# Kernel tuning notes

Measured on AMD Instinct MI355X. Metric: run time of the kernel, lower is better.

## Reference

```python
import jax, jax.numpy as jnp
import numpy as np

M, L, O, D, B = 512, 16, 32, 64, 16
GAMMA = 1.0 / (2.0 * D)  # RBF bandwidth ~ median sq-dist of randn data


def _rbf(X, Y):
    """Gaussian RBF kernel. X:[M,D]; Y:[M2,D] -> [M,M2] or Y:[B,L,D] -> [B,M,L]."""
    x2 = jnp.sum(X * X, axis=-1)
    y2 = jnp.sum(Y * Y, axis=-1)
    if Y.ndim == 3:
        d2 = x2[None, :, None] + y2[:, None, :] - 2.0 * jnp.einsum('md,bld->bml', X, Y)
    else:
        d2 = x2[:, None] + y2[None, :] - 2.0 * X @ Y.T
    return jnp.exp(-GAMMA * d2)


def setup_inputs() -> dict:
    key = jax.random.key(0)
    k1, k2, k3, k4 = jax.random.split(key, 4)
    inps = jax.random.normal(k1, (B, L, D), dtype=jnp.float32)
    nys_X = jax.random.normal(k2, (M, D), dtype=jnp.float32)
    nys_Y = jax.random.normal(k3, (M, D), dtype=jnp.float32)
    # xavier_uniform for (M*L, M*L)
    lim = float(np.sqrt(6.0 / (2 * M * L)))
    koopman = jax.random.uniform(k4, (M * L, M * L), dtype=jnp.float32, minval=-lim, maxval=lim)
    return {"inps": inps, "nys_X": nys_X, "nys_Y": nys_Y, "koopman": koopman}


def reference(inps, nys_X, nys_Y, koopman):
    scale = M ** (-0.5)
    KX = _rbf(nys_X, inps) * scale   # [B, M, L]
    KY = _rbf(nys_Y, nys_Y) * scale  # [M, M]
    out0 = KX.reshape(B, M * L)      # [B, M*L]

    def step(carry, _):
        nxt = carry @ koopman.T      # einsum('ij,bj->bi', G, out)
        return nxt, nxt

    _, outs = jax.lax.scan(step, out0, None, length=O)   # [O, B, M*L]
    outs = jnp.transpose(outs, (1, 2, 0)).reshape(B, M, L, O)
    outs = jnp.einsum('ij,bjlo->bilo', KY, outs)          # [B, M, L, O]
    outs = jnp.einsum('ja,bjlo->bloa', nys_Y, outs)       # [B, L, O, D]
    return outs
```

## Files before the change

kernel.cpp:

```cpp
#include <hip/hip_runtime.h>
#include <hip/hip_bf16.h>

#define M_  512
#define L_  16
#define O_  32
#define D_  64
#define B_  16
#define ML  8192
#define SLOT (B_*ML)

typedef __attribute__((ext_vector_type(8))) short short8;
typedef __attribute__((ext_vector_type(4))) float f32x4;

static constexpr float GAMMA = 1.0f / 128.0f;
static constexpr float SCALE = 0.0441941738241592f;

__device__ __forceinline__ float sqdiff4(const float4& x, const float4& y) {
    float dx = x.x - y.x, dy = x.y - y.y, dz = x.z - y.z, dw = x.w - y.w;
    return dx*dx + dy*dy + dz*dz + dw*dw;
}

__device__ __forceinline__ unsigned short f2bf(float x) {
    unsigned u = __float_as_uint(x);
    u = (u + 0x7FFFu + ((u >> 16) & 1u)) >> 16;
    return (unsigned short)u;
}

__global__ __launch_bounds__(256) void k_out0_dual(const float* __restrict__ inps,
                                                   const float* __restrict__ X,
                                                   float* __restrict__ S0,
                                                   unsigned short* __restrict__ C0) {
    int idx = blockIdx.x * 256 + threadIdx.x;
    int l = idx & (L_ - 1);
    int m = (idx >> 4) & (M_ - 1);
    int b = idx >> 13;
    const float* xr = X + m * D_;
    const float* yr = inps + (b * L_ + l) * D_;
    float d2 = 0.f;
#pragma unroll
    for (int d = 0; d < D_; d += 4) {
        float4 xv = *(const float4*)(xr + d);
        float4 yv = *(const float4*)(yr + d);
        d2 += sqdiff4(xv, yv);
    }
    float v = SCALE * expf(-GAMMA * d2);
    S0[idx] = v;
    C0[idx] = f2bf(v);
}

__global__ __launch_bounds__(256) void k_out0(const float* __restrict__ inps,
                                              const float* __restrict__ X,
                                              float* __restrict__ out0) {
    int idx = blockIdx.x * 256 + threadIdx.x;
    int l = idx & (L_ - 1);
    int m = (idx >> 4) & (M_ - 1);
    int b = idx >> 13;
    const float* xr = X + m * D_;
    const float* yr = inps + (b * L_ + l) * D_;
    float d2 = 0.f;
#pragma unroll
    for (int d = 0; d < D_; d += 4) {
        float4 xv = *(const float4*)(xr + d);
        float4 yv = *(const float4*)(yr + d);
        d2 += sqdiff4(xv, yv);
    }
    out0[idx] = SCALE * expf(-GAMMA * d2);
}

__global__ __launch_bounds__(256) void k_ky(const float* __restrict__ Y,
                                            float* __restrict__ KY) {
    int idx = blockIdx.x * 256 + threadIdx.x;
    int j = idx & (M_ - 1);
    int i = idx >> 9;
    const float* yi = Y + i * D_;
    const float* yj = Y + j * D_;
    float d2 = 0.f;
#pragma unroll
    for (int d = 0; d < D_; d += 4) {
        float4 a = *(const float4*)(yi + d);
        float4 b = *(const float4*)(yj + d);
        d2 += sqdiff4(a, b);
    }
    KY[idx] = SCALE * expf(-GAMMA * d2);
}

__global__ __launch_bounds__(256) void k_w(const float* __restrict__ KY,
                                           const float* __restrict__ Y,
                                           float* __restrict__ W) {
    int idx = blockIdx.x * 256 + threadIdx.x;
    int a = idx & (D_ - 1);
    int m = idx >> 6;
    float acc = 0.f;
    for (int j = 0; j < M_; ++j)
        acc = fmaf(KY[m * M_ + j], Y[j * D_ + a], acc);
    W[idx] = acc;
}


__global__ __launch_bounds__(512, 2) void k_step_first(const float* __restrict__ G,
                                                       unsigned short* __restrict__ Gp,
                                                       const unsigned short* __restrict__ Cin,
                                                       float* __restrict__ Sout,
                                                       unsigned short* __restrict__ Cout) {
    const int bx   = blockIdx.x;
    const int w    = threadIdx.x >> 6;
    const int lane = threadIdx.x & 63;
    const int r    = lane & 15;
    const int kk   = lane >> 4;
    const size_t kbase = (size_t)w * 1024 + kk * 8;
    const int mt0 = bx * 2, mt1 = bx * 2 + 1;

    const float* g0 = G + (size_t)(mt0 * 16 + r) * ML + kbase;
    const float* g1 = G + (size_t)(mt1 * 16 + r) * ML + kbase;
    unsigned short* gp0 = Gp + ((size_t)(mt0 * 256 + w * 32) * 64 + lane) * 8;
    unsigned short* gp1 = Gp + ((size_t)(mt1 * 256 + w * 32) * 64 + lane) * 8;
    const unsigned short* bp = Cin + (size_t)r * ML + kbase;

    const bool nt = (w < 4);
    f32x4 acc0 = {0.f, 0.f, 0.f, 0.f};
    f32x4 acc1 = {0.f, 0.f, 0.f, 0.f};
#pragma unroll 2
    for (int it = 0; it < 32; ++it) {
        short8 bv = *(const short8*)(bp + it * 32);
        f32x4 fa = __builtin_nontemporal_load((const f32x4*)(g0 + it * 32));
        f32x4 fb = __builtin_nontemporal_load((const f32x4*)(g0 + it * 32 + 4));
        union { short8 v; unsigned short u[8]; } oa;
        oa.u[0] = f2bf(fa.x); oa.u[1] = f2bf(fa.y); oa.u[2] = f2bf(fa.z); oa.u[3] = f2bf(fa.w);
        oa.u[4] = f2bf(fb.x); oa.u[5] = f2bf(fb.y); oa.u[6] = f2bf(fb.z); oa.u[7] = f2bf(fb.w);
        if (nt) __builtin_nontemporal_store(oa.v, (short8*)(gp0 + (size_t)it * 512));
        else    *(short8*)(gp0 + (size_t)it * 512) = oa.v;
        acc0 = __builtin_amdgcn_mfma_f32_16x16x32_bf16(oa.v, bv, acc0, 0, 0, 0);
        f32x4 fc = __builtin_nontemporal_load((const f32x4*)(g1 + it * 32));
        f32x4 fd = __builtin_nontemporal_load((const f32x4*)(g1 + it * 32 + 4));
        union { short8 v; unsigned short u[8]; } ob;
        ob.u[0] = f2bf(fc.x); ob.u[1] = f2bf(fc.y); ob.u[2] = f2bf(fc.z); ob.u[3] = f2bf(fc.w);
        ob.u[4] = f2bf(fd.x); ob.u[5] = f2bf(fd.y); ob.u[6] = f2bf(fd.z); ob.u[7] = f2bf(fd.w);
        if (nt) __builtin_nontemporal_store(ob.v, (short8*)(gp1 + (size_t)it * 512));
        else    *(short8*)(gp1 + (size_t)it * 512) = ob.v;
        acc1 = __builtin_amdgcn_mfma_f32_16x16x32_bf16(ob.v, bv, acc1, 0, 0, 0);
    }

    __shared__ float red[2][8][256];
    const int rbase = kk << 2;
#pragma unroll
    for (int q = 0; q < 4; ++q) {
        red[0][w][(rbase + q) * 16 + r] = acc0[q];
        red[1][w][(rbase + q) * 16 + r] = acc1[q];
    }
    __syncthreads();

    const int t = threadIdx.x;
    const int tl = t >> 8;
    const int t2 = t & 255;
    float s = 0.f;
#pragma unroll
    for (int p = 0; p < 8; ++p) s += red[tl][p][t2];
    const int b = t2 & 15;
    const int i = (bx << 5) + (tl << 4) + (t2 >> 4);
    Sout[(size_t)b * ML + i] = s;
    Cout[(size_t)b * ML + i] = f2bf(s);
}

template<bool NT>
__device__ __forceinline__ void step_loop(const unsigned short* ap0,
                                          const unsigned short* ap1,
                                          const unsigned short* bp,
                                          f32x4& acc0, f32x4& acc1) {
#pragma unroll 4
    for (int it = 0; it < 32; ++it) {
        short8 bv = *(const short8*)(bp + it * 32);
        short8 a0, a1;
        if constexpr (NT) {
            a0 = __builtin_nontemporal_load((const short8*)(ap0 + (size_t)it * 512));
            a1 = __builtin_nontemporal_load((const short8*)(ap1 + (size_t)it * 512));
        } else {
            a0 = *(const short8*)(ap0 + (size_t)it * 512);
            a1 = *(const short8*)(ap1 + (size_t)it * 512);
        }
        acc0 = __builtin_amdgcn_mfma_f32_16x16x32_bf16(a0, bv, acc0, 0, 0, 0);
        acc1 = __builtin_amdgcn_mfma_f32_16x16x32_bf16(a1, bv, acc1, 0, 0, 0);
    }
}

__global__ __launch_bounds__(512, 4) void k_step_next(const unsigned short* __restrict__ Gp,
                                                      const unsigned short* __restrict__ Cin,
                                                      float* __restrict__ Sout,
                                                      unsigned short* __restrict__ Cout) {
    const int bx   = blockIdx.x;
    const int w    = threadIdx.x >> 6;
    const int lane = threadIdx.x & 63;
    const int r    = lane & 15;
    const int kk   = lane >> 4;
    const size_t kbase = (size_t)w * 1024 + kk * 8;
    const int mt0 = bx * 2, mt1 = bx * 2 + 1;

    const unsigned short* ap0 = Gp + ((size_t)(mt0 * 256 + w * 32) * 64 + lane) * 8;
    const unsigned short* ap1 = Gp + ((size_t)(mt1 * 256 + w * 32) * 64 + lane) * 8;
    const unsigned short* bp  = Cin + (size_t)r * ML + kbase;

    f32x4 acc0 = {0.f, 0.f, 0.f, 0.f};
    f32x4 acc1 = {0.f, 0.f, 0.f, 0.f};
    if (w < 4) step_loop<true >(ap0, ap1, bp, acc0, acc1);
    else       step_loop<false>(ap0, ap1, bp, acc0, acc1);

    __shared__ float red[2][8][256];
    const int rbase = kk << 2;
#pragma unroll
    for (int q = 0; q < 4; ++q) {
        red[0][w][(rbase + q) * 16 + r] = acc0[q];
        red[1][w][(rbase + q) * 16 + r] = acc1[q];
    }
    __syncthreads();

    const int t = threadIdx.x;
    const int tl = t >> 8;
    const int t2 = t & 255;
    float s = 0.f;
#pragma unroll
    for (int p = 0; p < 8; ++p) s += red[tl][p][t2];
    const int b = t2 & 15;
    const int i = (bx << 5) + (tl << 4) + (t2 >> 4);
    Sout[(size_t)b * ML + i] = s;
    Cout[(size_t)b * ML + i] = f2bf(s);
}

__global__ __launch_bounds__(256) void k_step(const float* __restrict__ G,
                                              const float* __restrict__ carry,
                                              float* __restrict__ out) {
    const int i = blockIdx.x;
    const float* __restrict__ grow = G + (size_t)i * ML;
    float acc[B_];
#pragma unroll
    for (int b = 0; b < B_; ++b) acc[b] = 0.f;
    for (int j0 = threadIdx.x * 4; j0 < ML; j0 += 256 * 4) {
        float4 g = *(const float4*)(grow + j0);
#pragma unroll
        for (int b = 0; b < B_; ++b) {
            float4 c = *(const float4*)(carry + b * ML + j0);
            acc[b] = fmaf(g.x, c.x, fmaf(g.y, c.y, fmaf(g.z, c.z, fmaf(g.w, c.w, acc[b]))));
        }
    }
#pragma unroll
    for (int b = 0; b < B_; ++b) {
        float v = acc[b];
#pragma unroll
        for (int off = 32; off > 0; off >>= 1) v += __shfl_down(v, off, 64);
        acc[b] = v;
    }
    __shared__ float red2[4][B_];
    int lane = threadIdx.x & 63;
    int wv   = threadIdx.x >> 6;
    if (lane == 0) {
#pragma unroll
        for (int b = 0; b < B_; ++b) red2[wv][b] = acc[b];
    }
    __syncthreads();
    if (threadIdx.x < B_) {
        float v = red2[0][threadIdx.x] + red2[1][threadIdx.x] +
                  red2[2][threadIdx.x] + red2[3][threadIdx.x];
        out[threadIdx.x * ML + i] = v;
    }
}

__global__ __launch_bounds__(256) void k_final(const float* __restrict__ S,
                                               const float* __restrict__ W,
                                               float* __restrict__ out) {
    int t = blockIdx.x * 256 + threadIdx.x;
    int a = t & (D_ - 1);
    int w = t >> 6;
    int o = w & (O_ - 1);
    int bl = w >> 5;
    int l = bl & (L_ - 1);
    int b = bl >> 4;
    const float* slot = S + (size_t)(o + 1) * SLOT + b * ML;
    float acc = 0.f;
    for (int m = 0; m < M_; ++m)
        acc = fmaf(slot[m * L_ + l], W[m * D_ + a], acc);
    out[t] = acc;
}

extern "C" void kernel_launch(void* const* d_in, const int* in_sizes, int n_in,
                              void* d_out, int out_size, void* d_ws, size_t ws_size,
                              hipStream_t stream) {
    const float* inps    = (const float*)d_in[0];
    const float* nys_X   = (const float*)d_in[1];
    const float* nys_Y   = (const float*)d_in[2];
    const float* koopman = (const float*)d_in[3];
    float* out = (float*)d_out;

    const size_t GB_BYTES  = (size_t)ML * ML * 2;
    const size_t S_BYTES   = (size_t)33 * SLOT * 4;
    const size_t CB_BYTES  = (size_t)33 * SLOT * 2;
    const size_t KY_BYTES  = (size_t)M_ * M_ * 4;
    const size_t W_BYTES   = (size_t)M_ * D_ * 4;
    const size_t NEED_FAST = GB_BYTES + S_BYTES + CB_BYTES + KY_BYTES + W_BYTES;

    if (ws_size >= NEED_FAST) {
        unsigned short* Gp = (unsigned short*)d_ws;
        float*          S  = (float*)((char*)d_ws + GB_BYTES);
        unsigned short* Cb = (unsigned short*)((char*)S + S_BYTES);
        float*          KY = (float*)((char*)Cb + CB_BYTES);
        float*          W  = KY + M_ * M_;

        k_out0_dual<<<SLOT / 256, 256, 0, stream>>>(inps, nys_X, S, Cb);
        k_ky<<<(M_ * M_) / 256, 256, 0, stream>>>(nys_Y, KY);
        k_w<<<(M_ * D_) / 256, 256, 0, stream>>>(KY, nys_Y, W);

        k_step_first<<<256, 512, 0, stream>>>(koopman, Gp, Cb,
                                              S + (size_t)1 * SLOT,
                                              Cb + (size_t)1 * SLOT);
        for (int o = 2; o <= O_; ++o) {
            k_step_next<<<256, 512, 0, stream>>>(Gp,
                                                 Cb + (size_t)(o - 1) * SLOT,
                                                 S + (size_t)o * SLOT,
                                                 Cb + (size_t)o * SLOT);
        }
        k_final<<<(B_ * L_ * O_ * D_) / 256, 256, 0, stream>>>(S, W, out);
    } else {
        float* S  = (float*)d_ws;
        float* KY = S + (size_t)33 * SLOT;
        float* W  = KY + M_ * M_;

        k_out0<<<SLOT / 256, 256, 0, stream>>>(inps, nys_X, S);
        k_ky<<<(M_ * M_) / 256, 256, 0, stream>>>(nys_Y, KY);
        k_w<<<(M_ * D_) / 256, 256, 0, stream>>>(KY, nys_Y, W);
        for (int o = 1; o <= O_; ++o)
            k_step<<<ML, 256, 0, stream>>>(koopman, S + (size_t)(o - 1) * SLOT,
                                           S + (size_t)o * SLOT);
        k_final<<<(B_ * L_ * O_ * D_) / 256, 256, 0, stream>>>(S, W, out);
    }
}
```

Baseline: 1.082 ms.

## Drop nontemporal loads/stores in step kernels and restructure final projection kernel

Removes the nontemporal load/store split in the first and subsequent Koopman step kernels so every wave uses normal cached accesses to the bf16 Koopman matrix. This is meant to let the 128 MB packed matrix stay partly resident in the large last-level cache across the 31 repeated steps. Separately, the final projection kernel is rewritten so each block handles one (b,l) pair and each thread accumulates 8 output steps. Each loaded W value is reused 8 times and the launch shrinks to 256 blocks, which may lower parallelism for that kernel.

```diff
diff --git a/kernel.cpp b/kernel.cpp
--- a/kernel.cpp
+++ b/kernel.cpp
@@ -116,27 +116,24 @@
     unsigned short* gp1 = Gp + ((size_t)(mt1 * 256 + w * 32) * 64 + lane) * 8;
     const unsigned short* bp = Cin + (size_t)r * ML + kbase;
 
-    const bool nt = (w < 4);
     f32x4 acc0 = {0.f, 0.f, 0.f, 0.f};
     f32x4 acc1 = {0.f, 0.f, 0.f, 0.f};
 #pragma unroll 2
     for (int it = 0; it < 32; ++it) {
         short8 bv = *(const short8*)(bp + it * 32);
-        f32x4 fa = __builtin_nontemporal_load((const f32x4*)(g0 + it * 32));
-        f32x4 fb = __builtin_nontemporal_load((const f32x4*)(g0 + it * 32 + 4));
+        f32x4 fa = *(const f32x4*)(g0 + it * 32);
+        f32x4 fb = *(const f32x4*)(g0 + it * 32 + 4);
         union { short8 v; unsigned short u[8]; } oa;
         oa.u[0] = f2bf(fa.x); oa.u[1] = f2bf(fa.y); oa.u[2] = f2bf(fa.z); oa.u[3] = f2bf(fa.w);
         oa.u[4] = f2bf(fb.x); oa.u[5] = f2bf(fb.y); oa.u[6] = f2bf(fb.z); oa.u[7] = f2bf(fb.w);
-        if (nt) __builtin_nontemporal_store(oa.v, (short8*)(gp0 + (size_t)it * 512));
-        else    *(short8*)(gp0 + (size_t)it * 512) = oa.v;
+        *(short8*)(gp0 + (size_t)it * 512) = oa.v;
         acc0 = __builtin_amdgcn_mfma_f32_16x16x32_bf16(oa.v, bv, acc0, 0, 0, 0);
-        f32x4 fc = __builtin_nontemporal_load((const f32x4*)(g1 + it * 32));
-        f32x4 fd = __builtin_nontemporal_load((const f32x4*)(g1 + it * 32 + 4));
+        f32x4 fc = *(const f32x4*)(g1 + it * 32);
+        f32x4 fd = *(const f32x4*)(g1 + it * 32 + 4);
         union { short8 v; unsigned short u[8]; } ob;
         ob.u[0] = f2bf(fc.x); ob.u[1] = f2bf(fc.y); ob.u[2] = f2bf(fc.z); ob.u[3] = f2bf(fc.w);
         ob.u[4] = f2bf(fd.x); ob.u[5] = f2bf(fd.y); ob.u[6] = f2bf(fd.z); ob.u[7] = f2bf(fd.w);
-        if (nt) __builtin_nontemporal_store(ob.v, (short8*)(gp1 + (size_t)it * 512));
-        else    *(short8*)(gp1 + (size_t)it * 512) = ob.v;
+        *(short8*)(gp1 + (size_t)it * 512) = ob.v;
         acc1 = __builtin_amdgcn_mfma_f32_16x16x32_bf16(ob.v, bv, acc1, 0, 0, 0);
     }
 
@@ -159,27 +156,6 @@
     const int i = (bx << 5) + (tl << 4) + (t2 >> 4);
     Sout[(size_t)b * ML + i] = s;
     Cout[(size_t)b * ML + i] = f2bf(s);
-}
-
-template<bool NT>
-__device__ __forceinline__ void step_loop(const unsigned short* ap0,
-                                          const unsigned short* ap1,
-                                          const unsigned short* bp,
-                                          f32x4& acc0, f32x4& acc1) {
-#pragma unroll 4
-    for (int it = 0; it < 32; ++it) {
-        short8 bv = *(const short8*)(bp + it * 32);
-        short8 a0, a1;
-        if constexpr (NT) {
-            a0 = __builtin_nontemporal_load((const short8*)(ap0 + (size_t)it * 512));
-            a1 = __builtin_nontemporal_load((const short8*)(ap1 + (size_t)it * 512));
-        } else {
-            a0 = *(const short8*)(ap0 + (size_t)it * 512);
-            a1 = *(const short8*)(ap1 + (size_t)it * 512);
-        }
-        acc0 = __builtin_amdgcn_mfma_f32_16x16x32_bf16(a0, bv, acc0, 0, 0, 0);
-        acc1 = __builtin_amdgcn_mfma_f32_16x16x32_bf16(a1, bv, acc1, 0, 0, 0);
-    }
 }
 
 __global__ __launch_bounds__(512, 4) void k_step_next(const unsigned short* __restrict__ Gp,
@@ -200,8 +176,14 @@
 
     f32x4 acc0 = {0.f, 0.f, 0.f, 0.f};
     f32x4 acc1 = {0.f, 0.f, 0.f, 0.f};
-    if (w < 4) step_loop<true >(ap0, ap1, bp, acc0, acc1);
-    else       step_loop<false>(ap0, ap1, bp, acc0, acc1);
+#pragma unroll 4
+    for (int it = 0; it < 32; ++it) {
+        short8 bv = *(const short8*)(bp + it * 32);
+        short8 a0 = *(const short8*)(ap0 + (size_t)it * 512);
+        short8 a1 = *(const short8*)(ap1 + (size_t)it * 512);
+        acc0 = __builtin_amdgcn_mfma_f32_16x16x32_bf16(a0, bv, acc0, 0, 0, 0);
+        acc1 = __builtin_amdgcn_mfma_f32_16x16x32_bf16(a1, bv, acc1, 0, 0, 0);
+    }
 
     __shared__ float red[2][8][256];
     const int rbase = kk << 2;
@@ -262,21 +244,34 @@
     }
 }
 
-__global__ __launch_bounds__(256) void k_final(const float* __restrict__ S,
-                                               const float* __restrict__ W,
-                                               float* __restrict__ out) {
-    int t = blockIdx.x * 256 + threadIdx.x;
-    int a = t & (D_ - 1);
-    int w = t >> 6;
-    int o = w & (O_ - 1);
-    int bl = w >> 5;
-    int l = bl & (L_ - 1);
-    int b = bl >> 4;
-    const float* slot = S + (size_t)(o + 1) * SLOT + b * ML;
-    float acc = 0.f;
-    for (int m = 0; m < M_; ++m)
-        acc = fmaf(slot[m * L_ + l], W[m * D_ + a], acc);
-    out[t] = acc;
+__global__ __launch_bounds__(256) void k_final2(const float* __restrict__ S,
+                                                const float* __restrict__ W,
+                                                float* __restrict__ out) {
+    const int bid = blockIdx.x;
+    const int b = bid >> 4;
+    const int l = bid & 15;
+    const int a  = threadIdx.x & 63;
+    const int og = threadIdx.x >> 6;
+
+    float acc[8];
+#pragma unroll
+    for (int i = 0; i < 8; ++i) acc[i] = 0.f;
+
+    const float* sbase = S + (size_t)b * ML + l;
+    for (int m = 0; m < M_; ++m) {
+        float wa = W[m * D_ + a];
+#pragma unroll
+        for (int i = 0; i < 8; ++i) {
+            int o = og + 4 * i;
+            float sv = sbase[(size_t)(o + 1) * SLOT + m * L_];
+            acc[i] = fmaf(sv, wa, acc[i]);
+        }
+    }
+#pragma unroll
+    for (int i = 0; i < 8; ++i) {
+        int o = og + 4 * i;
+        out[((size_t)bid * O_ + o) * D_ + a] = acc[i];
+    }
 }
 
 extern "C" void kernel_launch(void* const* d_in, const int* in_sizes, int n_in,
@@ -315,7 +310,7 @@
                                                  S + (size_t)o * SLOT,
                                                  Cb + (size_t)o * SLOT);
         }
-        k_final<<<(B_ * L_ * O_ * D_) / 256, 256, 0, stream>>>(S, W, out);
+        k_final2<<<B_ * L_, 256, 0, stream>>>(S, W, out);
     } else {
         float* S  = (float*)d_ws;
         float* KY = S + (size_t)33 * SLOT;
@@ -327,6 +322,6 @@
         for (int o = 1; o <= O_; ++o)
             k_step<<<ML, 256, 0, stream>>>(koopman, S + (size_t)(o - 1) * SLOT,
                                            S + (size_t)o * SLOT);
-        k_final<<<(B_ * L_ * O_ * D_) / 256, 256, 0, stream>>>(S, W, out);
-    }
-}
+        k_final2<<<B_ * L_, 256, 0, stream>>>(S, W, out);
+    }
+}
```

New measurement: 1.076 ms. No clear change (-0.6%).
